# Optimization experiments

Hardware: AMD Instinct MI355X
Metric: run time of the kernel (lower is better)

The kernel has to match this reference:

```python
import jax, jax.numpy as jnp
import numpy as np
from jax.ops import segment_sum, segment_max

N = 38332
E = 1200000
C = 64
POI_LEN = 38333
CAT_LEN = 400
LAYERS = 5


def _glorot(key, shape):
    fan_in, fan_out = shape[0], shape[-1]
    lim = float(np.sqrt(6.0 / (fan_in + fan_out)))
    return jax.random.uniform(key, shape, jnp.float32, -lim, lim)


def gcn_conv(x, src, dst, ew, W, b):
    # PyG GCNConv: x@W, add self-loops (weight 1), symmetric norm, scatter-sum at dst
    h = x @ W  # [N, Cout]
    ar = jnp.arange(N, dtype=src.dtype)
    s = jnp.concatenate([src, ar])
    d = jnp.concatenate([dst, ar])
    w = jnp.concatenate([ew, jnp.ones((N,), ew.dtype)])
    deg = segment_sum(w, d, num_segments=N)
    dinv = jnp.where(deg > 0, jax.lax.rsqrt(jnp.maximum(deg, 1e-12)), 0.0)
    norm = dinv[s] * w * dinv[d]
    out = segment_sum(h[s] * norm[:, None], d, num_segments=N)
    return out + b


def graph_norm(x, w, b, alpha, eps=1e-5):
    mean = jnp.mean(x, axis=0, keepdims=True)
    out = x - alpha * mean
    var = jnp.mean(out * out, axis=0, keepdims=True)
    return out * jax.lax.rsqrt(var + eps) * w + b


def gat_conv(x, src, dst, W, att_src, att_dst, b):
    # PyG GATConv, heads=1, add_self_loops=True, negative_slope=0.2
    h = x @ W  # [N, C]
    ar = jnp.arange(N, dtype=src.dtype)
    s = jnp.concatenate([src, ar])
    d = jnp.concatenate([dst, ar])
    a_s = h @ att_src  # [N]
    a_d = h @ att_dst
    e = jax.nn.leaky_relu(a_s[s] + a_d[d], 0.2)  # [E+N]
    m = segment_max(e, d, num_segments=N)
    ex = jnp.exp(e - m[d])
    z = segment_sum(ex, d, num_segments=N)
    alpha = ex / (z[d] + 1e-16)
    out = segment_sum(h[s] * alpha[:, None], d, num_segments=N)
    return out + b


def setup_inputs() -> dict:
    key = jax.random.key(0)
    ks = jax.random.split(key, 32)
    inp = {
        'poi_idx': jax.random.randint(ks[0], (N,), 0, POI_LEN, jnp.int32),
        'cat_idx': jax.random.randint(ks[1], (N,), 0, CAT_LEN, jnp.int32),
        'feat': jax.random.normal(ks[2], (N, 3), jnp.float32),
        'edge_index': jax.random.randint(ks[3], (2, E), 0, N, jnp.int32),
        'weight': jax.random.uniform(ks[4], (E,), jnp.float32),
        'poi_emb': jax.random.normal(ks[5], (POI_LEN, 300), jnp.float32),
        'cat_emb': jax.random.normal(ks[6], (CAT_LEN, 100), jnp.float32),
        'W_in': _glorot(ks[7], (403, C)),
        'b_in': jnp.zeros((C,), jnp.float32),
        'gcn_W': jax.vmap(lambda k: _glorot(k, (C, C)))(jax.random.split(ks[8], LAYERS)),
        'gcn_b': jnp.zeros((LAYERS, C), jnp.float32),
        'gn_w': jnp.ones((LAYERS, C), jnp.float32),
        'gn_b': jnp.zeros((LAYERS, C), jnp.float32),
        'gn_a': jnp.ones((LAYERS, C), jnp.float32),
        'gat_W': jax.vmap(lambda k: _glorot(k, (C, C)))(jax.random.split(ks[9], LAYERS)),
        'gat_att_src': jax.random.normal(ks[10], (LAYERS, C), jnp.float32) * 0.1,
        'gat_att_dst': jax.random.normal(ks[11], (LAYERS, C), jnp.float32) * 0.1,
        'gat_b': jnp.zeros((LAYERS, C), jnp.float32),
        'W_out': _glorot(ks[12], (C, 1)),
        'b_out': jnp.zeros((1,), jnp.float32),
        'fc1_W': _glorot(ks[13], (N, 128)),
        'fc1_b': jnp.zeros((128,), jnp.float32),
        'fc2_W': _glorot(ks[14], (128, POI_LEN)),
        'fc2_b': jnp.zeros((POI_LEN,), jnp.float32),
    }
    return inp


def reference(poi_idx, cat_idx, feat, edge_index, weight, poi_emb, cat_emb,
              W_in, b_in, gcn_W, gcn_b, gn_w, gn_b, gn_a,
              gat_W, gat_att_src, gat_att_dst, gat_b,
              W_out, b_out, fc1_W, fc1_b, fc2_W, fc2_b):
    src, dst = edge_index[0], edge_index[1]
    lrelu = lambda v: jax.nn.leaky_relu(v, 0.01)  # nn.LeakyReLU default
    x = jnp.concatenate([poi_emb[poi_idx], cat_emb[cat_idx], feat], axis=1)  # [N,403]
    x = lrelu(gcn_conv(x, src, dst, weight, W_in, b_in))  # [N,64]
    for i in range(LAYERS):
        t = gcn_conv(x, src, dst, weight, gcn_W[i], gcn_b[i])
        t = lrelu(graph_norm(t, gn_w[i], gn_b[i], gn_a[i]))
        x = x + t
        t = gat_conv(x, src, dst, gat_W[i], gat_att_src[i], gat_att_dst[i], gat_b[i])
        t = lrelu(graph_norm(t, gn_w[i], gn_b[i], gn_a[i]))
        x = x + t
    x = lrelu(gcn_conv(x, src, dst, weight, W_out, b_out)).reshape(-1)  # [N]
    h = jax.nn.relu(x @ fc1_W + fc1_b)
    out = jax.nn.relu(h @ fc2_W + fc2_b)  # [POI_LEN]
    return out
```

## Files before the change

### kernel.cpp

```cpp
#include <hip/hip_runtime.h>
#include <hip/hip_fp16.h>

#define NN 38332
#define NE 1200000
#define POI 38333
#define NWG 128
#define CHUNK (NE/NWG)
#define SBLK 256

__device__ __forceinline__ float lrelu01(float v){ return v > 0.f ? v : 0.01f*v; }

__device__ __forceinline__ void load8(const __half* h, int s, int c8, float* f){
  uint4 q = *(const uint4*)((const __half*)h + (size_t)s*64 + c8);
  __half2 h0 = *(__half2*)&q.x, h1 = *(__half2*)&q.y, h2 = *(__half2*)&q.z, h3 = *(__half2*)&q.w;
  float2 r0 = __half22float2(h0), r1 = __half22float2(h1), r2 = __half22float2(h2), r3 = __half22float2(h3);
  f[0]=r0.x; f[1]=r0.y; f[2]=r1.x; f[3]=r1.y; f[4]=r2.x; f[5]=r2.y; f[6]=r3.x; f[7]=r3.y;
}
__device__ __forceinline__ void load8(const float* h, int s, int c8, float* f){
  float4 a = *(const float4*)(h + (size_t)s*64 + c8);
  float4 b = *(const float4*)(h + (size_t)s*64 + c8 + 4);
  f[0]=a.x; f[1]=a.y; f[2]=a.z; f[3]=a.w; f[4]=b.x; f[5]=b.y; f[6]=b.z; f[7]=b.w;
}

__global__ __launch_bounds__(1024) void k_hist(const int* __restrict__ dst,
                                               int* __restrict__ partial){
  __shared__ int hist[NN];
  for (int i = threadIdx.x; i < NN; i += 1024) hist[i] = 0;
  __syncthreads();
  int base = blockIdx.x*CHUNK;
  for (int k = threadIdx.x; k < CHUNK; k += 1024)
    atomicAdd(&hist[dst[base + k]], 1);
  __syncthreads();
  for (int i = threadIdx.x; i < NN; i += 1024)
    partial[(size_t)blockIdx.x*NN + i] = hist[i];
}

__global__ __launch_bounds__(256) void k_b1(int* __restrict__ partial, int* __restrict__ counts){
  int bin = blockIdx.x*256 + threadIdx.x;
  if (bin < NN){
    int run = 0;
    for (int wg = 0; wg < NWG; ++wg){
      int v = partial[(size_t)wg*NN + bin];
      partial[(size_t)wg*NN + bin] = run;
      run += v;
    }
    counts[bin] = run;
  }
}

__global__ __launch_bounds__(1024) void k_scan(const int* __restrict__ counts, int* rowptr){
  __shared__ int part[1024];
  int tid = threadIdx.x;
  const int per = (NN + 1023)/1024;
  int base = tid*per;
  int s = 0;
  for (int k = 0; k < per; k++){ int i = base + k; if (i < NN) s += counts[i]; }
  part[tid] = s;
  __syncthreads();
  for (int off = 1; off < 1024; off <<= 1){
    int v = (tid >= off) ? part[tid-off] : 0;
    __syncthreads();
    part[tid] += v;
    __syncthreads();
  }
  int run = (tid == 0) ? 0 : part[tid-1];
  for (int k = 0; k < per; k++){
    int i = base + k;
    if (i < NN){ rowptr[i] = run; run += counts[i]; }
  }
  if (tid == 1023) rowptr[NN] = run;
}

__global__ __launch_bounds__(1024) void k_scatter(const int* __restrict__ src,
                                                  const int* __restrict__ dst,
                                                  const float* __restrict__ ew,
                                                  const int* __restrict__ rowptr,
                                                  const int* __restrict__ partial,
                                                  int2* __restrict__ cw){
  __shared__ int cur[NN];
  for (int i = threadIdx.x; i < NN; i += 1024)
    cur[i] = rowptr[i] + partial[(size_t)blockIdx.x*NN + i];
  __syncthreads();
  int base = blockIdx.x*CHUNK;
  for (int k = threadIdx.x; k < CHUNK; k += 1024){
    int e = base + k;
    int d = dst[e];
    int pos = atomicAdd(&cur[d], 1);
    cw[pos] = make_int2(src[e], __float_as_int(ew[e]));
  }
}

__global__ __launch_bounds__(256) void k_dinv(const int* __restrict__ rowptr,
                                              const int2* __restrict__ cw,
                                              float* __restrict__ dinv){
  int lane = threadIdx.x & 63;
  int n = blockIdx.x*4 + (threadIdx.x >> 6);
  int beg = rowptr[n], end = rowptr[n+1];
  float s = 0.f;
  for (int e = beg + lane; e < end; e += 64) s += __int_as_float(cw[e].y);
  #pragma unroll
  for (int off = 32; off; off >>= 1) s += __shfl_xor(s, off);
  if (lane == 0) dinv[n] = rsqrtf(1.0f + s);
}

__global__ __launch_bounds__(256) void k_scale(const int* __restrict__ rowptr,
                                               const float* __restrict__ dinv,
                                               int2* __restrict__ cw){
  int lane = threadIdx.x & 63;
  int n = blockIdx.x*4 + (threadIdx.x >> 6);
  float dn = dinv[n];
  int beg = rowptr[n], end = rowptr[n+1];
  for (int e = beg + lane; e < end; e += 64){
    int2 p = cw[e];
    cw[e].y = __float_as_int(dinv[p.x]*__int_as_float(p.y)*dn);
  }
}

template<int K>
__global__ __launch_bounds__(256) void k_proj(const float* __restrict__ emb,
                                              const float* __restrict__ W,
                                              float* __restrict__ outp, int rows){
  int lane = threadIdx.x & 63;
  int base = __builtin_amdgcn_readfirstlane(blockIdx.x*32 + (threadIdx.x >> 6)*8);
  float acc[8] = {0.f,0.f,0.f,0.f,0.f,0.f,0.f,0.f};
  constexpr int NCH = (K + 63)/64;
  #pragma unroll
  for (int ch = 0; ch < NCH; ++ch){
    float Wreg[64];
    #pragma unroll
    for (int j = 0; j < 64; ++j)
      Wreg[j] = (ch*64 + j < K) ? W[(ch*64 + j)*64 + lane] : 0.f;
    #pragma unroll
    for (int r = 0; r < 8; ++r){
      int row = base + r;
      if (row < rows){
        const float* er = emb + (size_t)row*K + ch*64;
        #pragma unroll
        for (int j = 0; j < 64; ++j)
          if (ch*64 + j < K) acc[r] = fmaf(er[j], Wreg[j], acc[r]);
      }
    }
  }
  #pragma unroll
  for (int r = 0; r < 8; ++r){
    int row = base + r;
    if (row < rows) outp[(size_t)row*64 + lane] = acc[r];
  }
}

__global__ __launch_bounds__(256) void k_gather(const int* __restrict__ poi_idx,
                                                const int* __restrict__ cat_idx,
                                                const float* __restrict__ feat,
                                                const float* __restrict__ pproj,
                                                const float* __restrict__ cproj,
                                                const float* __restrict__ Wf,
                                                float* __restrict__ outh){
  int i = blockIdx.x*256 + threadIdx.x;
  int n = i >> 6, c = i & 63;
  float f0 = feat[n*3], f1 = feat[n*3+1], f2 = feat[n*3+2];
  float v = pproj[(size_t)poi_idx[n]*64 + c] + cproj[(size_t)cat_idx[n]*64 + c];
  v = fmaf(f0, Wf[c], v);
  v = fmaf(f1, Wf[64 + c], v);
  v = fmaf(f2, Wf[128 + c], v);
  outh[i] = v;
}

template<bool ATT, bool RESID>
__global__ __launch_bounds__(256) void k_lin64f(float* __restrict__ x,
                                                const float* __restrict__ t,
                                                const float* __restrict__ stats,
                                                const float* __restrict__ gb,
                                                const float* __restrict__ W,
                                                const float* __restrict__ att_src,
                                                const float* __restrict__ att_dst,
                                                __half* __restrict__ h,
                                                float* __restrict__ a_s,
                                                float* __restrict__ a_d){
  int lane = threadIdx.x & 63;
  int base = blockIdx.x*32 + (threadIdx.x >> 6)*8;
  float Wreg[64];
  #pragma unroll
  for (int j = 0; j < 64; ++j) Wreg[j] = W[j*64 + lane];
  float coef = 0.f, shift = 0.f, gbv = 0.f;
  if (RESID){
    coef  = stats[128 + lane];
    shift = stats[192 + lane];
    gbv   = gb[lane];
  }
  float as_l = 0.f, ad_l = 0.f;
  if (ATT){ as_l = att_src[lane]; ad_l = att_dst[lane]; }
  #pragma unroll
  for (int r = 0; r < 8; ++r){
    int row = base + r;
    if (row < NN){
      float xn = x[(size_t)row*64 + lane];
      if (RESID){
        float tv = t[(size_t)row*64 + lane];
        xn += lrelu01((tv - shift)*coef + gbv);
        x[(size_t)row*64 + lane] = xn;
      }
      int xi = __float_as_int(xn);
      float acc = 0.f;
      #pragma unroll
      for (int j = 0; j < 64; ++j)
        acc = fmaf(__int_as_float(__builtin_amdgcn_readlane(xi, j)), Wreg[j], acc);
      h[(size_t)row*64 + lane] = __float2half(acc);
      if (ATT){
        float s1 = acc*as_l, s2 = acc*ad_l;
        #pragma unroll
        for (int off = 32; off; off >>= 1){ s1 += __shfl_xor(s1, off); s2 += __shfl_xor(s2, off); }
        if (lane == 0){ a_s[row] = s1; a_d[row] = s2; }
      }
    }
  }
}

template<bool DO_LRELU, typename T>
__global__ __launch_bounds__(256) void k_gcn_prop(const T* __restrict__ h,
                                                  const int* __restrict__ rowptr,
                                                  const int2* __restrict__ cw,
                                                  const float* __restrict__ dinv,
                                                  const float* __restrict__ bias,
                                                  float* __restrict__ out){
  int lane = threadIdx.x & 63;
  int n = __builtin_amdgcn_readfirstlane(blockIdx.x*4 + (threadIdx.x >> 6));
  int beg = rowptr[n], end = rowptr[n+1];
  int deg = end - beg;
  int g  = lane >> 3;
  int c8 = (lane & 7) << 3;
  float acc[8] = {0.f,0.f,0.f,0.f,0.f,0.f,0.f,0.f};
  if (deg < 64){
    int sv = n; float wv = 0.f;
    if (lane < deg){
      int2 p = cw[beg + lane];
      sv = p.x; wv = __int_as_float(p.y);
    } else if (lane == deg){
      float di = dinv[n];
      wv = di*di;
    }
    int ne = deg + 1;
    int nit = (ne + 7) >> 3;
    float w0 = __shfl(wv, g);
    int  sj0 = __shfl(sv, g);
    float f0[8]; load8(h, sj0, c8, f0);
    for (int it = 1; it < nit; ++it){
      int ei = (it << 3) + g;
      float w1 = __shfl(wv, ei);
      int  sj1 = __shfl(sv, ei);
      float f1[8]; load8(h, sj1, c8, f1);
      #pragma unroll
      for (int j = 0; j < 8; ++j) acc[j] = fmaf(w0, f0[j], acc[j]);
      w0 = w1;
      #pragma unroll
      for (int j = 0; j < 8; ++j) f0[j] = f1[j];
    }
    #pragma unroll
    for (int j = 0; j < 8; ++j) acc[j] = fmaf(w0, f0[j], acc[j]);
  } else {
    {
      float di = dinv[n];
      float w = (g == 0) ? di*di : 0.f;
      float f[8]; load8(h, n, c8, f);
      #pragma unroll
      for (int j = 0; j < 8; ++j) acc[j] = fmaf(w, f[j], acc[j]);
    }
    int nit = (deg + 7) >> 3;
    for (int it = 0; it < nit; ++it){
      int ei = (it << 3) + g;
      int2 p = cw[beg + (ei < deg ? ei : 0)];
      float w = (ei < deg) ? __int_as_float(p.y) : 0.f;
      float f[8]; load8(h, p.x, c8, f);
      #pragma unroll
      for (int j = 0; j < 8; ++j) acc[j] = fmaf(w, f[j], acc[j]);
    }
  }
  #pragma unroll
  for (int m = 8; m < 64; m <<= 1){
    #pragma unroll
    for (int j = 0; j < 8; ++j) acc[j] += __shfl_xor(acc[j], m);
  }
  if (lane < 8){
    int cb = lane << 3;
    float4 b0 = *(const float4*)&bias[cb];
    float4 b1 = *(const float4*)&bias[cb + 4];
    float o[8] = {acc[0]+b0.x, acc[1]+b0.y, acc[2]+b0.z, acc[3]+b0.w,
                  acc[4]+b1.x, acc[5]+b1.y, acc[6]+b1.z, acc[7]+b1.w};
    if (DO_LRELU){
      #pragma unroll
      for (int j = 0; j < 8; ++j) o[j] = lrelu01(o[j]);
    }
    *(float4*)&out[(size_t)n*64 + cb]     = make_float4(o[0],o[1],o[2],o[3]);
    *(float4*)&out[(size_t)n*64 + cb + 4] = make_float4(o[4],o[5],o[6],o[7]);
  }
}

__global__ __launch_bounds__(256) void k_gat_prop(const __half* __restrict__ h,
                                                  const int* __restrict__ rowptr,
                                                  const int2* __restrict__ cw,
                                                  const float* __restrict__ a_s,
                                                  const float* __restrict__ a_d,
                                                  const float* __restrict__ bias,
                                                  float* __restrict__ out){
  int lane = threadIdx.x & 63;
  int n = __builtin_amdgcn_readfirstlane(blockIdx.x*4 + (threadIdx.x >> 6));
  int beg = rowptr[n], end = rowptr[n+1];
  int deg = end - beg;
  float ad = a_d[n];
  float se = a_s[n] + ad; se = se > 0.f ? se : 0.2f*se;
  if (deg <= 64){
    int s = 0; float v = -1e30f;
    if (lane < deg){
      s = cw[beg + lane].x;
      v = a_s[s] + ad; v = v > 0.f ? v : 0.2f*v;
    }
    float m = fmaxf(se, v);
    #pragma unroll
    for (int off = 32; off; off >>= 1) m = fmaxf(m, __shfl_xor(m, off));
    float ev = (lane < deg) ? __expf(v - m) : 0.f;
    float z = ev;
    #pragma unroll
    for (int off = 32; off; off >>= 1) z += __shfl_xor(z, off);
    float es = __expf(se - m);
    z += es;
    float zinv = 1.0f/(z + 1e-16f);
    int g = lane >> 3, c8 = (lane & 7) << 3;
    float acc[8] = {0.f,0.f,0.f,0.f,0.f,0.f,0.f,0.f};
    { float f[8]; load8(h, n, c8, f);
      float w = (g == 0) ? es : 0.f;
      #pragma unroll
      for (int j = 0; j < 8; ++j) acc[j] = fmaf(w, f[j], acc[j]);
    }
    int nit = (deg + 7) >> 3;
    if (nit > 0){
      float w0 = __shfl(ev, g);
      int  sj0 = __shfl(s,  g);
      float f0[8]; load8(h, sj0, c8, f0);
      for (int it = 1; it < nit; ++it){
        int ei = (it << 3) + g;
        float w1 = __shfl(ev, ei);
        int  sj1 = __shfl(s,  ei);
        float f1[8]; load8(h, sj1, c8, f1);
        #pragma unroll
        for (int j = 0; j < 8; ++j) acc[j] = fmaf(w0, f0[j], acc[j]);
        w0 = w1;
        #pragma unroll
        for (int j = 0; j < 8; ++j) f0[j] = f1[j];
      }
      #pragma unroll
      for (int j = 0; j < 8; ++j) acc[j] = fmaf(w0, f0[j], acc[j]);
    }
    #pragma unroll
    for (int mm = 8; mm < 64; mm <<= 1){
      #pragma unroll
      for (int j = 0; j < 8; ++j) acc[j] += __shfl_xor(acc[j], mm);
    }
    if (lane < 8){
      int cb = lane << 3;
      float4 b0 = *(const float4*)&bias[cb];
      float4 b1 = *(const float4*)&bias[cb + 4];
      float o[8] = {fmaf(acc[0],zinv,b0.x), fmaf(acc[1],zinv,b0.y), fmaf(acc[2],zinv,b0.z), fmaf(acc[3],zinv,b0.w),
                    fmaf(acc[4],zinv,b1.x), fmaf(acc[5],zinv,b1.y), fmaf(acc[6],zinv,b1.z), fmaf(acc[7],zinv,b1.w)};
      *(float4*)&out[(size_t)n*64 + cb]     = make_float4(o[0],o[1],o[2],o[3]);
      *(float4*)&out[(size_t)n*64 + cb + 4] = make_float4(o[4],o[5],o[6],o[7]);
    }
  } else {
    float m = se;
    for (int e = beg + lane; e < end; e += 64){
      float v = a_s[cw[e].x] + ad; v = v > 0.f ? v : 0.2f*v;
      m = fmaxf(m, v);
    }
    #pragma unroll
    for (int off = 32; off; off >>= 1) m = fmaxf(m, __shfl_xor(m, off));
    float z = 0.f;
    for (int e = beg + lane; e < end; e += 64){
      float v = a_s[cw[e].x] + ad; v = v > 0.f ? v : 0.2f*v;
      z += __expf(v - m);
    }
    #pragma unroll
    for (int off = 32; off; off >>= 1) z += __shfl_xor(z, off);
    float es = __expf(se - m);
    z += es;
    float zinv = 1.0f/(z + 1e-16f);
    float acc = es*(float)h[(size_t)n*64 + lane];
    for (int e = beg; e < end; ++e){
      int sj = cw[e].x;
      float v = a_s[sj] + ad; v = v > 0.f ? v : 0.2f*v;
      acc = fmaf(__expf(v - m), (float)h[(size_t)sj*64 + lane], acc);
    }
    out[(size_t)n*64 + lane] = acc*zinv + bias[lane];
  }
}

__global__ __launch_bounds__(256) void k_colstats(const float* __restrict__ t,
                                                  float* __restrict__ pstats){
  int lane = threadIdx.x & 63;
  int sub  = threadIdx.x >> 6;
  float s = 0.f, s2 = 0.f;
  for (int n = blockIdx.x*4 + sub; n < NN; n += gridDim.x*4){
    float v = t[(size_t)n*64 + lane];
    s += v; s2 = fmaf(v, v, s2);
  }
  __shared__ float ls[256], ls2[256];
  ls[threadIdx.x] = s; ls2[threadIdx.x] = s2;
  __syncthreads();
  if (threadIdx.x < 64){
    s  = ls[threadIdx.x]  + ls[threadIdx.x+64]  + ls[threadIdx.x+128]  + ls[threadIdx.x+192];
    s2 = ls2[threadIdx.x] + ls2[threadIdx.x+64] + ls2[threadIdx.x+128] + ls2[threadIdx.x+192];
    pstats[blockIdx.x*128 + threadIdx.x]      = s;
    pstats[blockIdx.x*128 + 64 + threadIdx.x] = s2;
  }
}

__global__ __launch_bounds__(256) void k_chan(const float* __restrict__ pstats,
                                              const float* __restrict__ gw,
                                              const float* __restrict__ ga,
                                              float* __restrict__ stats){
  int lane = threadIdx.x & 63, w = threadIdx.x >> 6;
  float s = 0.f, s2 = 0.f;
  for (int blk = w*(SBLK/4); blk < (w+1)*(SBLK/4); ++blk){
    s  += pstats[blk*128 + lane];
    s2 += pstats[blk*128 + 64 + lane];
  }
  __shared__ float ls[256], ls2[256];
  ls[threadIdx.x] = s; ls2[threadIdx.x] = s2;
  __syncthreads();
  if (threadIdx.x < 64){
    int c = threadIdx.x;
    s  = ls[c]  + ls[c+64]  + ls[c+128]  + ls[c+192];
    s2 = ls2[c] + ls2[c+64] + ls2[c+128] + ls2[c+192];
    const float invN = 1.0f/(float)NN;
    float m  = s*invN, ms = s2*invN, a = ga[c];
    float var = ms - m*m*a*(2.0f - a);
    stats[128 + c] = rsqrtf(var + 1e-5f)*gw[c];
    stats[192 + c] = a*m;
  }
}

__global__ __launch_bounds__(256) void k_outlinf(const float* __restrict__ x,
                                                 const float* __restrict__ t,
                                                 const float* __restrict__ stats,
                                                 const float* __restrict__ gb,
                                                 const float* __restrict__ Wout,
                                                 float* __restrict__ h1){
  int lane = threadIdx.x & 63, wave = threadIdx.x >> 6;
  int n = blockIdx.x*4 + wave;
  float coef  = stats[128 + lane];
  float shift = stats[192 + lane];
  float xn = x[(size_t)n*64 + lane];
  float tv = t[(size_t)n*64 + lane];
  xn += lrelu01((tv - shift)*coef + gb[lane]);
  float v = xn*Wout[lane];
  #pragma unroll
  for (int off = 32; off; off >>= 1) v += __shfl_xor(v, off);
  if (lane == 0) h1[n] = v;
}

__global__ __launch_bounds__(256) void k_prop1(const float* __restrict__ h1,
                                               const int* __restrict__ rowptr,
                                               const int2* __restrict__ cw,
                                               const float* __restrict__ dinv,
                                               const float* __restrict__ b_out,
                                               float* __restrict__ xs){
  int lane = threadIdx.x & 63;
  int n = blockIdx.x*32 + (threadIdx.x >> 6)*8 + (lane >> 3);
  bool ok = n < NN;
  int beg = ok ? rowptr[n] : 0;
  int end = ok ? rowptr[n+1] : 0;
  float acc = 0.f;
  for (int e = beg + (lane & 7); e < end; e += 8){
    int2 p = cw[e];
    acc = fmaf(__int_as_float(p.y), h1[p.x], acc);
  }
  acc += __shfl_xor(acc, 1);
  acc += __shfl_xor(acc, 2);
  acc += __shfl_xor(acc, 4);
  if (ok && (lane & 7) == 0){
    float di = dinv[n];
    xs[n] = lrelu01(acc + di*di*h1[n] + b_out[0]);
  }
}

__global__ __launch_bounds__(256) void k_fc1(const float* __restrict__ xs,
                                             const float* __restrict__ W,
                                             float* __restrict__ pfc){
  int j = threadIdx.x & 127, half = threadIdx.x >> 7;
  float acc = 0.f;
  for (int n = blockIdx.x*2 + half; n < NN; n += gridDim.x*2)
    acc = fmaf(xs[n], W[(size_t)n*128 + j], acc);
  __shared__ float ls[256];
  ls[threadIdx.x] = acc;
  __syncthreads();
  if (threadIdx.x < 128) pfc[blockIdx.x*128 + j] = ls[j] + ls[128 + j];
}

__global__ __launch_bounds__(256) void k_fc2(const float* __restrict__ pfc,
                                             const float* __restrict__ fc1_b,
                                             const float* __restrict__ W2,
                                             const float* __restrict__ b2,
                                             float* __restrict__ out){
  __shared__ float hs[128];
  if (threadIdx.x < 128){
    float v = fc1_b[threadIdx.x];
    for (int blk = 0; blk < 128; ++blk) v += pfc[blk*128 + threadIdx.x];
    hs[threadIdx.x] = v > 0.f ? v : 0.f;
  }
  __syncthreads();
  int p = blockIdx.x*256 + threadIdx.x;
  if (p < POI){
    float acc = b2[p];
    #pragma unroll
    for (int j = 0; j < 128; j++) acc = fmaf(hs[j], W2[(size_t)j*POI + p], acc);
    out[p] = acc > 0.f ? acc : 0.f;
  }
}

extern "C" void kernel_launch(void* const* d_in, const int* in_sizes, int n_in,
                              void* d_out, int out_size, void* d_ws, size_t ws_size,
                              hipStream_t stream) {
  const int*   poi_idx = (const int*)d_in[0];
  const int*   cat_idx = (const int*)d_in[1];
  const float* feat    = (const float*)d_in[2];
  const int*   eidx    = (const int*)d_in[3];
  const int*   src     = eidx;
  const int*   dst     = eidx + NE;
  const float* ew      = (const float*)d_in[4];
  const float* poi_emb = (const float*)d_in[5];
  const float* cat_emb = (const float*)d_in[6];
  const float* W_in    = (const float*)d_in[7];
  const float* b_in    = (const float*)d_in[8];
  const float* gcn_W   = (const float*)d_in[9];
  const float* gcn_b   = (const float*)d_in[10];
  const float* gn_w    = (const float*)d_in[11];
  const float* gn_b    = (const float*)d_in[12];
  const float* gn_a    = (const float*)d_in[13];
  const float* gat_W   = (const float*)d_in[14];
  const float* att_s   = (const float*)d_in[15];
  const float* att_d   = (const float*)d_in[16];
  const float* gat_b   = (const float*)d_in[17];
  const float* W_out   = (const float*)d_in[18];
  const float* b_out   = (const float*)d_in[19];
  const float* fc1_W   = (const float*)d_in[20];
  const float* fc1_b   = (const float*)d_in[21];
  const float* fc2_W   = (const float*)d_in[22];
  const float* fc2_b   = (const float*)d_in[23];
  float* out = (float*)d_out;

  char* p = (char*)d_ws;
  auto alloc = [&](size_t bytes){ void* r = (void*)p; p += (bytes + 255) & ~(size_t)255; return r; };
  float*  x      = (float*) alloc((size_t)NN*64*4);
  float*  t      = (float*) alloc((size_t)NN*64*4);
  __half* h      = (__half*)alloc((size_t)NN*64*2);
  int*    partial= (int*)   alloc((size_t)NWG*NN*4);
  float*  pproj  = (float*) partial;
  float*  cproj  = (float*) alloc((size_t)400*64*4);
  int2*   cw     = (int2*)  alloc((size_t)NE*8);
  float*  dinv   = (float*) alloc(NN*4);
  int*    counts = (int*)   alloc(NN*4);
  int*    rowptr = (int*)   alloc((NN+1)*4);
  float*  a_s    = (float*) alloc(NN*4);
  float*  a_d    = (float*) alloc(NN*4);
  float*  pstats = (float*) alloc((size_t)SBLK*128*4);
  float*  stats  = (float*) alloc(256*4);
  float*  h1     = (float*) alloc(NN*4);
  float*  xs     = (float*) alloc(NN*4);
  float*  pfc    = (float*) alloc(128*128*4);

  const int G_N   = (NN + 255)/256;
  const int G_W4  = NN/4;
  const int G_L   = (NN + 31)/32;
  const int G_PJ  = (POI + 31)/32;
  const int G_EL  = NN*64/256;
  const int G_P1  = (NN + 31)/32;

  k_hist   <<<NWG, 1024, 0, stream>>>(dst, partial);
  k_b1     <<<G_N, 256, 0, stream>>>(partial, counts);
  k_scan   <<<1, 1024, 0, stream>>>(counts, rowptr);
  k_scatter<<<NWG, 1024, 0, stream>>>(src, dst, ew, rowptr, partial, cw);
  k_dinv   <<<G_W4, 256, 0, stream>>>(rowptr, cw, dinv);
  k_scale  <<<G_W4, 256, 0, stream>>>(rowptr, dinv, cw);

  k_proj<300><<<G_PJ, 256, 0, stream>>>(poi_emb, W_in, pproj, POI);
  k_proj<100><<<13, 256, 0, stream>>>(cat_emb, W_in + 300*64, cproj, 400);
  k_gather<<<G_EL, 256, 0, stream>>>(poi_idx, cat_idx, feat, pproj, cproj, W_in + 400*64, t);
  k_gcn_prop<true, float><<<G_W4, 256, 0, stream>>>(t, rowptr, cw, dinv, b_in, x);

  for (int i = 0; i < 5; i++){
    if (i == 0)
      k_lin64f<false,false><<<G_L, 256, 0, stream>>>(x, nullptr, nullptr, nullptr,
                                                     gcn_W, nullptr, nullptr, h, nullptr, nullptr);
    else
      k_lin64f<false,true><<<G_L, 256, 0, stream>>>(x, t, stats, gn_b + (i-1)*64,
                                                    gcn_W + i*4096, nullptr, nullptr, h, nullptr, nullptr);
    k_gcn_prop<false, __half><<<G_W4, 256, 0, stream>>>(h, rowptr, cw, dinv, gcn_b + i*64, t);
    k_colstats<<<SBLK, 256, 0, stream>>>(t, pstats);
    k_chan<<<1, 256, 0, stream>>>(pstats, gn_w + i*64, gn_a + i*64, stats);
    k_lin64f<true,true><<<G_L, 256, 0, stream>>>(x, t, stats, gn_b + i*64,
                                                 gat_W + i*4096, att_s + i*64, att_d + i*64, h, a_s, a_d);
    k_gat_prop<<<G_W4, 256, 0, stream>>>(h, rowptr, cw, a_s, a_d, gat_b + i*64, t);
    k_colstats<<<SBLK, 256, 0, stream>>>(t, pstats);
    k_chan<<<1, 256, 0, stream>>>(pstats, gn_w + i*64, gn_a + i*64, stats);
  }

  k_outlinf<<<G_W4, 256, 0, stream>>>(x, t, stats, gn_b + 4*64, W_out, h1);
  k_prop1<<<G_P1, 256, 0, stream>>>(h1, rowptr, cw, dinv, b_out, xs);
  k_fc1<<<128, 256, 0, stream>>>(xs, fc1_W, pfc);
  k_fc2<<<(POI + 255)/256, 256, 0, stream>>>(pfc, fc1_b, fc2_W, fc2_b, out);
}
```

Before: 1.012 ms.

## Store conv outputs in fp16 and split POI projection into two halves

The intermediate conv output buffer t becomes fp16 for the GCN and GAT propagation layers, so the propagation stores and the colstats, lin64f and outlinf reads move half the bytes. Separately, the 300-wide POI embedding projection is split into two 150-column launches writing two partial buffers, which the gather kernel then sums. The split lowers per-thread register pressure and may raise occupancy, at the cost of an extra launch and an extra gather read. The fp16 storage of t adds rounding error before the graph-norm statistics.

After: 1.027 ms. Within noise of the previous version (+1.5%).

```diff
diff --git a/kernel.cpp b/kernel.cpp
--- a/kernel.cpp
+++ b/kernel.cpp
@@ -20,6 +20,19 @@
   float4 a = *(const float4*)(h + (size_t)s*64 + c8);
   float4 b = *(const float4*)(h + (size_t)s*64 + c8 + 4);
   f[0]=a.x; f[1]=a.y; f[2]=a.z; f[3]=a.w; f[4]=b.x; f[5]=b.y; f[6]=b.z; f[7]=b.w;
+}
+__device__ __forceinline__ void store8(float* out, int n, int cb, const float* o){
+  *(float4*)&out[(size_t)n*64 + cb]     = make_float4(o[0],o[1],o[2],o[3]);
+  *(float4*)&out[(size_t)n*64 + cb + 4] = make_float4(o[4],o[5],o[6],o[7]);
+}
+__device__ __forceinline__ void store8(__half* out, int n, int cb, const float* o){
+  __half2 q0 = __floats2half2_rn(o[0], o[1]);
+  __half2 q1 = __floats2half2_rn(o[2], o[3]);
+  __half2 q2 = __floats2half2_rn(o[4], o[5]);
+  __half2 q3 = __floats2half2_rn(o[6], o[7]);
+  uint4 q;
+  q.x = *(unsigned*)&q0; q.y = *(unsigned*)&q1; q.z = *(unsigned*)&q2; q.w = *(unsigned*)&q3;
+  *(uint4*)((__half*)out + (size_t)n*64 + cb) = q;
 }
 
 __global__ __launch_bounds__(1024) void k_hist(const int* __restrict__ dst,
@@ -116,28 +129,28 @@
   }
 }
 
-template<int K>
+template<int KC, int KS>
 __global__ __launch_bounds__(256) void k_proj(const float* __restrict__ emb,
                                               const float* __restrict__ W,
                                               float* __restrict__ outp, int rows){
   int lane = threadIdx.x & 63;
   int base = __builtin_amdgcn_readfirstlane(blockIdx.x*32 + (threadIdx.x >> 6)*8);
   float acc[8] = {0.f,0.f,0.f,0.f,0.f,0.f,0.f,0.f};
-  constexpr int NCH = (K + 63)/64;
+  constexpr int NCH = (KC + 63)/64;
   #pragma unroll
   for (int ch = 0; ch < NCH; ++ch){
     float Wreg[64];
     #pragma unroll
     for (int j = 0; j < 64; ++j)
-      Wreg[j] = (ch*64 + j < K) ? W[(ch*64 + j)*64 + lane] : 0.f;
+      Wreg[j] = (ch*64 + j < KC) ? W[(ch*64 + j)*64 + lane] : 0.f;
     #pragma unroll
     for (int r = 0; r < 8; ++r){
       int row = base + r;
       if (row < rows){
-        const float* er = emb + (size_t)row*K + ch*64;
+        const float* er = emb + (size_t)row*KS + ch*64;
         #pragma unroll
         for (int j = 0; j < 64; ++j)
-          if (ch*64 + j < K) acc[r] = fmaf(er[j], Wreg[j], acc[r]);
+          if (ch*64 + j < KC) acc[r] = fmaf(er[j], Wreg[j], acc[r]);
       }
     }
   }
@@ -151,14 +164,16 @@
 __global__ __launch_bounds__(256) void k_gather(const int* __restrict__ poi_idx,
                                                 const int* __restrict__ cat_idx,
                                                 const float* __restrict__ feat,
-                                                const float* __restrict__ pproj,
+                                                const float* __restrict__ pp1,
+                                                const float* __restrict__ pp2,
                                                 const float* __restrict__ cproj,
                                                 const float* __restrict__ Wf,
                                                 float* __restrict__ outh){
   int i = blockIdx.x*256 + threadIdx.x;
   int n = i >> 6, c = i & 63;
+  int pi = poi_idx[n];
   float f0 = feat[n*3], f1 = feat[n*3+1], f2 = feat[n*3+2];
-  float v = pproj[(size_t)poi_idx[n]*64 + c] + cproj[(size_t)cat_idx[n]*64 + c];
+  float v = pp1[(size_t)pi*64 + c] + pp2[(size_t)pi*64 + c] + cproj[(size_t)cat_idx[n]*64 + c];
   v = fmaf(f0, Wf[c], v);
   v = fmaf(f1, Wf[64 + c], v);
   v = fmaf(f2, Wf[128 + c], v);
@@ -167,7 +182,7 @@
 
 template<bool ATT, bool RESID>
 __global__ __launch_bounds__(256) void k_lin64f(float* __restrict__ x,
-                                                const float* __restrict__ t,
+                                                const __half* __restrict__ t,
                                                 const float* __restrict__ stats,
                                                 const float* __restrict__ gb,
                                                 const float* __restrict__ W,
@@ -195,7 +210,7 @@
     if (row < NN){
       float xn = x[(size_t)row*64 + lane];
       if (RESID){
-        float tv = t[(size_t)row*64 + lane];
+        float tv = __half2float(t[(size_t)row*64 + lane]);
         xn += lrelu01((tv - shift)*coef + gbv);
         x[(size_t)row*64 + lane] = xn;
       }
@@ -215,13 +230,13 @@
   }
 }
 
-template<bool DO_LRELU, typename T>
-__global__ __launch_bounds__(256) void k_gcn_prop(const T* __restrict__ h,
+template<bool DO_LRELU, typename TIN, typename TOUT>
+__global__ __launch_bounds__(256) void k_gcn_prop(const TIN* __restrict__ h,
                                                   const int* __restrict__ rowptr,
                                                   const int2* __restrict__ cw,
                                                   const float* __restrict__ dinv,
                                                   const float* __restrict__ bias,
-                                                  float* __restrict__ out){
+                                                  TOUT* __restrict__ out){
   int lane = threadIdx.x & 63;
   int n = __builtin_amdgcn_readfirstlane(blockIdx.x*4 + (threadIdx.x >> 6));
   int beg = rowptr[n], end = rowptr[n+1];
@@ -289,8 +304,7 @@
       #pragma unroll
       for (int j = 0; j < 8; ++j) o[j] = lrelu01(o[j]);
     }
-    *(float4*)&out[(size_t)n*64 + cb]     = make_float4(o[0],o[1],o[2],o[3]);
-    *(float4*)&out[(size_t)n*64 + cb + 4] = make_float4(o[4],o[5],o[6],o[7]);
+    store8(out, n, cb, o);
   }
 }
 
@@ -300,7 +314,7 @@
                                                   const float* __restrict__ a_s,
                                                   const float* __restrict__ a_d,
                                                   const float* __restrict__ bias,
-                                                  float* __restrict__ out){
+                                                  __half* __restrict__ out){
   int lane = threadIdx.x & 63;
   int n = __builtin_amdgcn_readfirstlane(blockIdx.x*4 + (threadIdx.x >> 6));
   int beg = rowptr[n], end = rowptr[n+1];
@@ -360,8 +374,7 @@
       float4 b1 = *(const float4*)&bias[cb + 4];
       float o[8] = {fmaf(acc[0],zinv,b0.x), fmaf(acc[1],zinv,b0.y), fmaf(acc[2],zinv,b0.z), fmaf(acc[3],zinv,b0.w),
                     fmaf(acc[4],zinv,b1.x), fmaf(acc[5],zinv,b1.y), fmaf(acc[6],zinv,b1.z), fmaf(acc[7],zinv,b1.w)};
-      *(float4*)&out[(size_t)n*64 + cb]     = make_float4(o[0],o[1],o[2],o[3]);
-      *(float4*)&out[(size_t)n*64 + cb + 4] = make_float4(o[4],o[5],o[6],o[7]);
+      store8(out, n, cb, o);
     }
   } else {
     float m = se;
@@ -387,17 +400,17 @@
       float v = a_s[sj] + ad; v = v > 0.f ? v : 0.2f*v;
       acc = fmaf(__expf(v - m), (float)h[(size_t)sj*64 + lane], acc);
     }
-    out[(size_t)n*64 + lane] = acc*zinv + bias[lane];
-  }
-}
-
-__global__ __launch_bounds__(256) void k_colstats(const float* __restrict__ t,
+    out[(size_t)n*64 + lane] = __float2half(acc*zinv + bias[lane]);
+  }
+}
+
+__global__ __launch_bounds__(256) void k_colstats(const __half* __restrict__ t,
                                                   float* __restrict__ pstats){
   int lane = threadIdx.x & 63;
   int sub  = threadIdx.x >> 6;
   float s = 0.f, s2 = 0.f;
   for (int n = blockIdx.x*4 + sub; n < NN; n += gridDim.x*4){
-    float v = t[(size_t)n*64 + lane];
+    float v = __half2float(t[(size_t)n*64 + lane]);
     s += v; s2 = fmaf(v, v, s2);
   }
   __shared__ float ls[256], ls2[256];
@@ -437,7 +450,7 @@
 }
 
 __global__ __launch_bounds__(256) void k_outlinf(const float* __restrict__ x,
-                                                 const float* __restrict__ t,
+                                                 const __half* __restrict__ t,
                                                  const float* __restrict__ stats,
                                                  const float* __restrict__ gb,
                                                  const float* __restrict__ Wout,
@@ -447,7 +460,7 @@
   float coef  = stats[128 + lane];
   float shift = stats[192 + lane];
   float xn = x[(size_t)n*64 + lane];
-  float tv = t[(size_t)n*64 + lane];
+  float tv = __half2float(t[(size_t)n*64 + lane]);
   xn += lrelu01((tv - shift)*coef + gb[lane]);
   float v = xn*Wout[lane];
   #pragma unroll
@@ -548,10 +561,12 @@
   char* p = (char*)d_ws;
   auto alloc = [&](size_t bytes){ void* r = (void*)p; p += (bytes + 255) & ~(size_t)255; return r; };
   float*  x      = (float*) alloc((size_t)NN*64*4);
-  float*  t      = (float*) alloc((size_t)NN*64*4);
+  float*  t32    = (float*) alloc((size_t)NN*64*4);
+  __half* t      = (__half*)alloc((size_t)NN*64*2);
   __half* h      = (__half*)alloc((size_t)NN*64*2);
   int*    partial= (int*)   alloc((size_t)NWG*NN*4);
-  float*  pproj  = (float*) partial;
+  float*  pproj1 = (float*) partial;
+  float*  pproj2 = (float*) alloc((size_t)POI*64*4);
   float*  cproj  = (float*) alloc((size_t)400*64*4);
   int2*   cw     = (int2*)  alloc((size_t)NE*8);
   float*  dinv   = (float*) alloc(NN*4);
@@ -579,10 +594,11 @@
   k_dinv   <<<G_W4, 256, 0, stream>>>(rowptr, cw, dinv);
   k_scale  <<<G_W4, 256, 0, stream>>>(rowptr, dinv, cw);
 
-  k_proj<300><<<G_PJ, 256, 0, stream>>>(poi_emb, W_in, pproj, POI);
-  k_proj<100><<<13, 256, 0, stream>>>(cat_emb, W_in + 300*64, cproj, 400);
-  k_gather<<<G_EL, 256, 0, stream>>>(poi_idx, cat_idx, feat, pproj, cproj, W_in + 400*64, t);
-  k_gcn_prop<true, float><<<G_W4, 256, 0, stream>>>(t, rowptr, cw, dinv, b_in, x);
+  k_proj<150,300><<<G_PJ, 256, 0, stream>>>(poi_emb,       W_in,          pproj1, POI);
+  k_proj<150,300><<<G_PJ, 256, 0, stream>>>(poi_emb + 150, W_in + 150*64, pproj2, POI);
+  k_proj<100,100><<<13, 256, 0, stream>>>(cat_emb, W_in + 300*64, cproj, 400);
+  k_gather<<<G_EL, 256, 0, stream>>>(poi_idx, cat_idx, feat, pproj1, pproj2, cproj, W_in + 400*64, t32);
+  k_gcn_prop<true, float, float><<<G_W4, 256, 0, stream>>>(t32, rowptr, cw, dinv, b_in, x);
 
   for (int i = 0; i < 5; i++){
     if (i == 0)
@@ -591,7 +607,7 @@
     else
       k_lin64f<false,true><<<G_L, 256, 0, stream>>>(x, t, stats, gn_b + (i-1)*64,
                                                     gcn_W + i*4096, nullptr, nullptr, h, nullptr, nullptr);
-    k_gcn_prop<false, __half><<<G_W4, 256, 0, stream>>>(h, rowptr, cw, dinv, gcn_b + i*64, t);
+    k_gcn_prop<false, __half, __half><<<G_W4, 256, 0, stream>>>(h, rowptr, cw, dinv, gcn_b + i*64, t);
     k_colstats<<<SBLK, 256, 0, stream>>>(t, pstats);
     k_chan<<<1, 256, 0, stream>>>(pstats, gn_w + i*64, gn_a + i*64, stats);
     k_lin64f<true,true><<<G_L, 256, 0, stream>>>(x, t, stats, gn_b + i*64,
```
